# Optimization experiments

Measured on AMD Instinct MI355X. Metric: run time of the kernel, lower is better.

The kernel has to match this reference:

```python
import jax, jax.numpy as jnp
import numpy as np

HEADS = 16
EMBED = 1024
HEAD_DIM = EMBED // HEADS

def _split_heads(x):
    b, n, _ = x.shape
    return x.reshape(b, n, HEADS, HEAD_DIM).transpose(0, 2, 1, 3)  # b h n d

def _merge_heads(x):
    b, h, n, d = x.shape
    return x.transpose(0, 2, 1, 3).reshape(b, n, h * d)

def _attn(q_in, kv_in, Wq, bq, Wk, bk, Wv, bv, Wo, bo):
    q = _split_heads(q_in @ Wq + bq)
    k = _split_heads(kv_in @ Wk + bk)
    v = _split_heads(kv_in @ Wv + bv)
    e = jnp.einsum('bhqd,bhkd->bhqk', q, k) * (HEAD_DIM ** -0.5)
    a = jax.nn.softmax(e, axis=-1)
    o = jnp.einsum('bhqk,bhkd->bhqd', a, v)
    return _merge_heads(o) @ Wo + bo

def _layernorm(x, g, b, eps=1e-5):
    mu = jnp.mean(x, axis=-1, keepdims=True)
    var = jnp.var(x, axis=-1, keepdims=True)
    return (x - mu) * jax.lax.rsqrt(var + eps) * g + b

def setup_inputs() -> dict:
    key = jax.random.key(0)
    ks = jax.random.split(key, 20)
    s = 0.02
    d = {
        'temp_features': jax.random.normal(ks[0], (2, 2048, EMBED), jnp.float32),
        'spat_features': jax.random.normal(ks[1], (2, 2048, EMBED), jnp.float32),
    }
    names = ['t2s_Wq', 't2s_Wk', 't2s_Wv', 't2s_Wo', 's2t_Wq', 's2t_Wk', 's2t_Wv', 's2t_Wo']
    for i, nm in enumerate(names):
        d[nm] = jax.random.normal(ks[2 + i], (EMBED, EMBED), jnp.float32) * s
        d[nm.replace('W', 'b')] = jnp.zeros((EMBED,), jnp.float32)
    d['ln_g'] = jnp.ones((EMBED,), jnp.float32)
    d['ln_b'] = jnp.zeros((EMBED,), jnp.float32)
    return d

def reference(temp_features, spat_features,
              t2s_Wq, t2s_bq, t2s_Wk, t2s_bk, t2s_Wv, t2s_bv, t2s_Wo, t2s_bo,
              s2t_Wq, s2t_bq, s2t_Wk, s2t_bk, s2t_Wv, s2t_bv, s2t_Wo, s2t_bo,
              ln_g, ln_b):
    # t2s: queries from spat, keys/values from temp; residual = spat
    t2s = _attn(spat_features, temp_features, t2s_Wq, t2s_bq, t2s_Wk, t2s_bk,
                t2s_Wv, t2s_bv, t2s_Wo, t2s_bo)
    t2s_out = _layernorm(spat_features + t2s, ln_g, ln_b)
    # s2t: queries from temp, keys/values from spat; residual = temp
    s2t = _attn(temp_features, spat_features, s2t_Wq, s2t_bq, s2t_Wk, s2t_bk,
                s2t_Wv, s2t_bv, s2t_Wo, s2t_bo)
    s2t_out = _layernorm(temp_features + s2t, ln_g, ln_b)
    return (s2t_out, t2s_out)
```

## Files before the change

kernel.cpp:

```cpp
#include <hip/hip_runtime.h>
#include <stdint.h>

#define SEQ 2048
#define EMB 1024
#define NROWS 4096

typedef __bf16 bf16x8 __attribute__((ext_vector_type(8)));
typedef float f32x4 __attribute__((ext_vector_type(4)));
typedef unsigned short ushort8 __attribute__((ext_vector_type(8)));

__device__ __forceinline__ unsigned short f2bf(float f) {
  unsigned int u = __float_as_uint(f);
  u += 0x7fffu + ((u >> 16) & 1u);
  return (unsigned short)(u >> 16);
}

__device__ __forceinline__ float bf2f(unsigned short h) {
  return __uint_as_float((unsigned int)h << 16);
}

__device__ __forceinline__ f32x4 mfma16(bf16x8 a, bf16x8 b, f32x4 c) {
  return __builtin_amdgcn_mfma_f32_16x16x32_bf16(a, b, c, 0, 0, 0);
}

__device__ __forceinline__ void async_load16(const void* g, void* l) {
  auto gp = reinterpret_cast<__attribute__((address_space(1))) void*>(
      reinterpret_cast<uintptr_t>(g));
  auto lp = reinterpret_cast<__attribute__((address_space(3))) void*>(
      reinterpret_cast<uintptr_t>(l));
  __builtin_amdgcn_global_load_lds(gp, lp, 16, 0, 0);
}

__global__ __launch_bounds__(256) void prep(const float* __restrict__ t,
                                            const float* __restrict__ s,
                                            unsigned short* __restrict__ tb,
                                            unsigned short* __restrict__ sb,
                                            const float* __restrict__ W0,
                                            const float* __restrict__ W1,
                                            const float* __restrict__ W2,
                                            const float* __restrict__ W3,
                                            const float* __restrict__ W4,
                                            const float* __restrict__ W5,
                                            const float* __restrict__ W6,
                                            const float* __restrict__ W7,
                                            unsigned short* __restrict__ Wt) {
  const int bx = blockIdx.x;
  if (bx < 8192) {
    int i = bx * 256 + threadIdx.x;
    const float* x; unsigned short* y;
    if (i < NROWS * EMB / 4) { x = t; y = tb; }
    else { x = s; y = sb; i -= NROWS * EMB / 4; }
    float4 v = ((const float4*)x)[i];
    ushort4 o;
    o.x = f2bf(v.x); o.y = f2bf(v.y); o.z = f2bf(v.z); o.w = f2bf(v.w);
    ((ushort4*)y)[i] = o;
    return;
  }
  const int e = bx - 8192;
  const int z = e >> 8, tt = e & 255;
  const float* Ws[8] = {W0, W1, W2, W3, W4, W5, W6, W7};
  const float* W = Ws[z];
  unsigned short* dst = Wt + ((size_t)z << 20);
  __shared__ unsigned short tile[64][65];
  const int n0 = (tt & 15) * 64, k0 = (tt >> 4) * 64;
#pragma unroll
  for (int i = 0; i < 16; ++i) {
    const int ee = i * 256 + threadIdx.x;
    const int kk = ee >> 6, nn = ee & 63;
    tile[kk][nn] = f2bf(W[(size_t)(k0 + kk) * EMB + n0 + nn]);
  }
  __syncthreads();
#pragma unroll
  for (int i = 0; i < 16; ++i) {
    const int ee = i * 256 + threadIdx.x;
    const int nn = ee >> 6, kk = ee & 63;
    dst[(size_t)(n0 + nn) * EMB + k0 + kk] = tile[kk][nn];
  }
}

__device__ __forceinline__ void gemm_core64(const unsigned short* __restrict__ A,
                                            const unsigned short* __restrict__ Bt,
                                            int m0, int bt0,
                                            unsigned short* As, unsigned short* Bs,
                                            f32x4 (&acc)[4][4]) {
  const int tid = threadIdx.x;
  const int w = tid >> 6, lane = tid & 63;
  const int quad = lane >> 4, l16 = lane & 15;
  const int wm = w & 1, wn = w >> 1;
  const int sw8 = l16 & 7;

  const int srow = lane >> 3, p8 = lane & 7;
  const unsigned short* Ag[4];
  const unsigned short* Bg[4];
#pragma unroll
  for (int i = 0; i < 4; ++i) {
    const int r = w * 32 + i * 8 + srow;
    Ag[i] = A + (size_t)(m0 + r) * EMB + ((p8 ^ (r & 7)) * 8);
    Bg[i] = Bt + (size_t)(bt0 + r) * EMB + ((p8 ^ (r & 7)) * 8);
  }
  unsigned short* AsB[4];
  unsigned short* BsB[4];
#pragma unroll
  for (int i = 0; i < 4; ++i) {
    AsB[i] = As + (w * 32 + i * 8) * 64;
    BsB[i] = Bs + (w * 32 + i * 8) * 64;
  }

  for (int kk = 0; kk < EMB; kk += 64) {
    __syncthreads();
#pragma unroll
    for (int i = 0; i < 4; ++i) {
      async_load16(Ag[i] + kk, AsB[i]);
      async_load16(Bg[i] + kk, BsB[i]);
    }
    __syncthreads();
#pragma unroll
    for (int h = 0; h < 2; ++h) {
      bf16x8 af[4], bfr[4];
#pragma unroll
      for (int im = 0; im < 4; ++im)
        af[im] = *(const bf16x8*)(As + (wm * 64 + im * 16 + l16) * 64 +
                                  (((h * 4 + quad) ^ sw8) * 8));
#pragma unroll
      for (int in = 0; in < 4; ++in)
        bfr[in] = *(const bf16x8*)(Bs + (wn * 64 + in * 16 + l16) * 64 +
                                   (((h * 4 + quad) ^ sw8) * 8));
#pragma unroll
      for (int im = 0; im < 4; ++im)
#pragma unroll
        for (int in = 0; in < 4; ++in)
          acc[im][in] = mfma16(af[im], bfr[in], acc[im][in]);
    }
  }
}

__global__ __launch_bounds__(256, 3) void gemm_qkv(const unsigned short* __restrict__ tempb,
                                                   const unsigned short* __restrict__ spatb,
                                                   const unsigned short* __restrict__ Wt,
                                                   const float* __restrict__ bq0,
                                                   const float* __restrict__ bk0,
                                                   const float* __restrict__ bv0,
                                                   const float* __restrict__ bq1,
                                                   const float* __restrict__ bk1,
                                                   const float* __restrict__ bv1,
                                                   unsigned short* __restrict__ Qb,
                                                   unsigned short* __restrict__ Kb,
                                                   unsigned short* __restrict__ Vtb) {
  __shared__ alignas(16) unsigned short As[128 * 64];
  __shared__ alignas(16) unsigned short Bs[128 * 64];
  const int idx = blockIdx.x >> 3;
  const int dir = idx / 3, kind = idx - dir * 3;
  const int n0 = (blockIdx.x & 7) * 128;
  const unsigned short* A =
      (dir == 0) ? (kind == 0 ? tempb : spatb) : (kind == 0 ? spatb : tempb);
  const float* bias = (dir == 0) ? (kind == 0 ? bq0 : (kind == 1 ? bk0 : bv0))
                                 : (kind == 0 ? bq1 : (kind == 1 ? bk1 : bv1));

  f32x4 acc[4][4] = {};
  gemm_core64(A, Wt + ((size_t)(dir * 4 + kind) << 20), blockIdx.y * 128, n0, As, Bs, acc);

  const int tid = threadIdx.x;
  const int w = tid >> 6, lane = tid & 63;
  const int quad = lane >> 4, l16 = lane & 15;
  const int wm = w & 1, wn = w >> 1;
  const int rowb = blockIdx.y * 128 + wm * 64;
  const size_t dof = (size_t)dir * NROWS * EMB;

  if (kind == 2) {
    unsigned short* Vt = Vtb + dof;
#pragma unroll
    for (int in = 0; in < 4; ++in) {
      const int col = n0 + wn * 64 + in * 16 + l16;
      const int h = col >> 6, d = col & 63;
      const float bvv = bias[col];
#pragma unroll
      for (int im = 0; im < 4; ++im) {
        const int row = rowb + im * 16 + quad * 4;
        const int b = row >> 11, key = row & 2047;
        ushort4 o;
        o.x = f2bf(acc[im][in][0] + bvv);
        o.y = f2bf(acc[im][in][1] + bvv);
        o.z = f2bf(acc[im][in][2] + bvv);
        o.w = f2bf(acc[im][in][3] + bvv);
        *(ushort4*)(Vt + ((size_t)(b * 16 + h) * 64 + d) * SEQ + key) = o;
      }
    }
  } else {
    unsigned short* out = ((kind == 0) ? Qb : Kb) + dof;
    const float scale = (kind == 0) ? 0.18033688011112042f : 1.0f;
#pragma unroll
    for (int in = 0; in < 4; ++in) {
      const int col = n0 + wn * 64 + in * 16 + l16;
      const float bvv = bias[col];
#pragma unroll
      for (int im = 0; im < 4; ++im)
#pragma unroll
        for (int r = 0; r < 4; ++r) {
          const int row = rowb + im * 16 + quad * 4 + r;
          out[(size_t)row * EMB + col] = f2bf((acc[im][in][r] + bvv) * scale);
        }
    }
  }
}

__global__ __launch_bounds__(256, 3) void gemm_o(const unsigned short* __restrict__ Ob,
                                                 const unsigned short* __restrict__ Wt,
                                                 const float* __restrict__ bo0,
                                                 const float* __restrict__ bo1,
                                                 const float* __restrict__ temp,
                                                 const float* __restrict__ spat,
                                                 unsigned short* __restrict__ projb) {
  __shared__ alignas(16) unsigned short As[128 * 64];
  __shared__ alignas(16) unsigned short Bs[128 * 64];
  const int dir = blockIdx.x >> 3;
  const int n0 = (blockIdx.x & 7) * 128;
  const size_t dof = (size_t)dir * NROWS * EMB;
  const float* bias = dir ? bo1 : bo0;
  const float* resid = dir ? spat : temp;

  f32x4 acc[4][4] = {};
  gemm_core64(Ob + dof, Wt + ((size_t)(dir * 4 + 3) << 20), blockIdx.y * 128, n0, As, Bs,
              acc);

  const int tid = threadIdx.x;
  const int w = tid >> 6, lane = tid & 63;
  const int quad = lane >> 4, l16 = lane & 15;
  const int wm = w & 1, wn = w >> 1;
  const int rowb = blockIdx.y * 128 + wm * 64;
  unsigned short* outb = projb + dof;
#pragma unroll
  for (int in = 0; in < 4; ++in) {
    const int col = n0 + wn * 64 + in * 16 + l16;
    const float bvv = bias[col];
#pragma unroll
    for (int im = 0; im < 4; ++im)
#pragma unroll
      for (int r = 0; r < 4; ++r) {
        const int row = rowb + im * 16 + quad * 4 + r;
        const size_t off = (size_t)row * EMB + col;
        outb[off] = f2bf(acc[im][in][r] + bvv + resid[off]);
      }
  }
}

__global__ __launch_bounds__(256, 4) void flash_attn(const unsigned short* __restrict__ Qall,
                                                     const unsigned short* __restrict__ Kall,
                                                     const unsigned short* __restrict__ Vtall,
                                                     unsigned short* __restrict__ Oall) {
  __shared__ alignas(16) unsigned short Ks[2][64 * 64];
  __shared__ alignas(16) unsigned short Vs[64 * 64];
  __shared__ alignas(16) unsigned short Ps[4][2048];

  const int tid = threadIdx.x;
  const int w = tid >> 6, lane = tid & 63;
  const int quad = lane >> 4, l16 = lane & 15;
  const int phys = blockIdx.x + (blockIdx.y << 4);
  const int xcd = phys & 7, slot = phys >> 3;
  const int bxv = slot & 15;
  const int byv = (xcd << 3) + (slot >> 4);
  const int dir = byv >> 5, bh = byv & 31;
  const int b = bh >> 4, h = bh & 15;
  const size_t dof = (size_t)dir * NROWS * EMB;
  const unsigned short* Q = Qall + dof;
  const unsigned short* K = Kall + dof;
  const unsigned short* Vt = Vtall + dof;
  unsigned short* O = Oall + dof;
  const int q0 = bxv * 128 + w * 32;

  bf16x8 qf[2][2];
#pragma unroll
  for (int qh = 0; qh < 2; ++qh) {
    const unsigned short* Qrow = Q + (size_t)(b * SEQ + q0 + qh * 16 + l16) * EMB + h * 64;
    qf[qh][0] = *(const bf16x8*)(Qrow + quad * 8);
    qf[qh][1] = *(const bf16x8*)(Qrow + 32 + quad * 8);
  }

  bf16x8 onesf;
#pragma unroll
  for (int i = 0; i < 8; ++i) onesf[i] = (__bf16)1.0f;

  f32x4 oaccT[2][4] = {};
  f32x4 rs[2] = {};
  unsigned short* pw = &Ps[w][0];
  const int swz = (l16 & 7) << 1;
  const int sw8 = l16 & 7;

  const int r8 = lane >> 3, p8 = lane & 7;
  const int kr0 = w * 16 + r8, kr1 = kr0 + 8;
  const unsigned short* Ksrc0 = K + (size_t)(b * SEQ + kr0) * EMB + h * 64 + ((p8 ^ (kr0 & 7)) * 8);
  const unsigned short* Ksrc1 = K + (size_t)(b * SEQ + kr1) * EMB + h * 64 + ((p8 ^ (kr1 & 7)) * 8);
  const unsigned short* Vsrc0 = Vt + ((size_t)bh * 64 + kr0) * SEQ + ((p8 ^ (kr0 & 7)) * 8);
  const unsigned short* Vsrc1 = Vt + ((size_t)bh * 64 + kr1) * SEQ + ((p8 ^ (kr1 & 7)) * 8);
  unsigned short* KsW0 = &Ks[0][0] + (w * 16) * 64;
  unsigned short* KsW1 = &Ks[0][0] + (w * 16 + 8) * 64;
  unsigned short* VsW0 = Vs + (w * 16) * 64;
  unsigned short* VsW1 = Vs + (w * 16 + 8) * 64;

  async_load16(Ksrc0, KsW0);
  async_load16(Ksrc1, KsW1);
  async_load16(Vsrc0, VsW0);
  async_load16(Vsrc1, VsW1);
  asm volatile("s_waitcnt vmcnt(0)" ::: "memory");
  __builtin_amdgcn_s_barrier();
  asm volatile("" ::: "memory");

  int cur = 0;
  for (int kt = 0; kt < SEQ; kt += 64) {
    const bool more = (kt + 64 < SEQ);
    const int nb = cur ^ 1;
    if (more) {
      async_load16(Ksrc0 + (size_t)(kt + 64) * EMB, KsW0 + nb * 4096);
      async_load16(Ksrc1 + (size_t)(kt + 64) * EMB, KsW1 + nb * 4096);
    }

    const unsigned short* KsC = &Ks[cur][0];

#pragma unroll
    for (int g = 0; g < 4; ++g) {
      const int key = g * 16 + l16;
      bf16x8 kf0 = *(const bf16x8*)(KsC + key * 64 + ((quad ^ sw8) * 8));
      bf16x8 kf1 = *(const bf16x8*)(KsC + key * 64 + (((4 + quad) ^ sw8) * 8));
      const int kb = 4 * g + quad;
#pragma unroll
      for (int qh = 0; qh < 2; ++qh) {
        f32x4 z = {};
        z = mfma16(kf0, qf[qh][0], z);
        z = mfma16(kf1, qf[qh][1], z);
        uint2 pk;
        pk.x = (__float_as_uint(__builtin_amdgcn_exp2f(z[0])) >> 16) |
               (__float_as_uint(__builtin_amdgcn_exp2f(z[1])) & 0xffff0000u);
        pk.y = (__float_as_uint(__builtin_amdgcn_exp2f(z[2])) >> 16) |
               (__float_as_uint(__builtin_amdgcn_exp2f(z[3])) & 0xffff0000u);
        *(uint2*)(pw + (qh * 16 + l16) * 64 + ((kb ^ swz) << 2)) = pk;
      }
    }
    asm volatile("" ::: "memory");
    bf16x8 pb[2][2];
#pragma unroll
    for (int qh = 0; qh < 2; ++qh) {
      const int qrow = qh * 16 + l16;
      pb[qh][0] = *(const bf16x8*)(pw + qrow * 64 + (((2 * quad) ^ swz) << 2));
      pb[qh][1] = *(const bf16x8*)(pw + qrow * 64 + (((8 + 2 * quad) ^ swz) << 2));
      rs[qh] = mfma16(onesf, pb[qh][1], mfma16(onesf, pb[qh][0], rs[qh]));
    }
    asm volatile("" ::: "memory");

    if (more) asm volatile("s_waitcnt vmcnt(2)" ::: "memory");
    else      asm volatile("s_waitcnt vmcnt(0)" ::: "memory");
    __builtin_amdgcn_s_barrier();
    asm volatile("" ::: "memory");

#pragma unroll
    for (int dg = 0; dg < 4; ++dg) {
      const int dd = dg * 16 + l16;
      bf16x8 v0 = *(const bf16x8*)(Vs + dd * 64 + ((quad ^ sw8) * 8));
      bf16x8 v1 = *(const bf16x8*)(Vs + dd * 64 + (((4 + quad) ^ sw8) * 8));
#pragma unroll
      for (int qh = 0; qh < 2; ++qh) {
        oaccT[qh][dg] = mfma16(v0, pb[qh][0], oaccT[qh][dg]);
        oaccT[qh][dg] = mfma16(v1, pb[qh][1], oaccT[qh][dg]);
      }
    }
    asm volatile("" ::: "memory");

    if (more) {
      __builtin_amdgcn_s_barrier();
      async_load16(Vsrc0 + (kt + 64), VsW0);
      async_load16(Vsrc1 + (kt + 64), VsW1);
      asm volatile("s_waitcnt vmcnt(2)" ::: "memory");
      __builtin_amdgcn_s_barrier();
      asm volatile("" ::: "memory");
    }
    cur ^= 1;
  }

#pragma unroll
  for (int qh = 0; qh < 2; ++qh) {
    const float inv = 1.0f / rs[qh][0];
#pragma unroll
    for (int dg = 0; dg < 4; ++dg) {
      uint2 pk;
      pk.x = (unsigned int)f2bf(oaccT[qh][dg][0] * inv) |
             ((unsigned int)f2bf(oaccT[qh][dg][1] * inv) << 16);
      pk.y = (unsigned int)f2bf(oaccT[qh][dg][2] * inv) |
             ((unsigned int)f2bf(oaccT[qh][dg][3] * inv) << 16);
      const int kb = 4 * dg + quad;
      *(uint2*)(pw + l16 * 64 + ((kb ^ swz) << 2)) = pk;
    }
    asm volatile("" ::: "memory");
    const int qq = lane >> 2, cc = lane & 3;
    const int swq = (qq & 7) << 1;
    ushort8 r0 = *(const ushort8*)(pw + qq * 64 + (((4 * cc) ^ swq) << 2));
    ushort8 r1 = *(const ushort8*)(pw + qq * 64 + (((4 * cc + 2) ^ swq) << 2));
    unsigned short* Orow = O + (size_t)(b * SEQ + q0 + qh * 16 + qq) * EMB + h * 64 + cc * 16;
    *(ushort8*)(Orow) = r0;
    *(ushort8*)(Orow + 8) = r1;
    asm volatile("" ::: "memory");
  }
}

__global__ __launch_bounds__(256) void ln_k(const unsigned short* __restrict__ X,
                                            const float* __restrict__ g,
                                            const float* __restrict__ bb,
                                            float* __restrict__ out) {
  const int row = blockIdx.x;
  const int tid = threadIdx.x;
  const ushort4 hv = ((const ushort4*)(X + (size_t)row * EMB))[tid];
  float4 v;
  v.x = bf2f(hv.x); v.y = bf2f(hv.y); v.z = bf2f(hv.z); v.w = bf2f(hv.w);
  float s = v.x + v.y + v.z + v.w;
  float s2 = v.x * v.x + v.y * v.y + v.z * v.z + v.w * v.w;
#pragma unroll
  for (int o = 32; o > 0; o >>= 1) {
    s += __shfl_down(s, o);
    s2 += __shfl_down(s2, o);
  }
  __shared__ float ws[4], ws2[4];
  if ((tid & 63) == 0) { ws[tid >> 6] = s; ws2[tid >> 6] = s2; }
  __syncthreads();
  const float S = ws[0] + ws[1] + ws[2] + ws[3];
  const float S2 = ws2[0] + ws2[1] + ws2[2] + ws2[3];
  const float mu = S * (1.f / EMB);
  const float inv = rsqrtf(S2 * (1.f / EMB) - mu * mu + 1e-5f);
  const float4 gv = ((const float4*)g)[tid];
  const float4 bv = ((const float4*)bb)[tid];
  float4 o4;
  o4.x = (v.x - mu) * inv * gv.x + bv.x;
  o4.y = (v.y - mu) * inv * gv.y + bv.y;
  o4.z = (v.z - mu) * inv * gv.z + bv.z;
  o4.w = (v.w - mu) * inv * gv.w + bv.w;
  ((float4*)(out + (size_t)row * EMB))[tid] = o4;
}

extern "C" void kernel_launch(void* const* d_in, const int* in_sizes, int n_in,
                              void* d_out, int out_size, void* d_ws, size_t ws_size,
                              hipStream_t stream) {
  const float* temp = (const float*)d_in[0];
  const float* spat = (const float*)d_in[1];
  const float* lng = (const float*)d_in[18];
  const float* lnb = (const float*)d_in[19];
  float* out = (float*)d_out;

  char* base = (char*)d_ws;
  unsigned short* tempb = (unsigned short*)(base + ((size_t)0 << 20));
  unsigned short* spatb = (unsigned short*)(base + ((size_t)8 << 20));
  unsigned short* Wt = (unsigned short*)(base + ((size_t)16 << 20));
  unsigned short* Qb = (unsigned short*)(base + ((size_t)32 << 20));
  unsigned short* Kb = (unsigned short*)(base + ((size_t)48 << 20));
  unsigned short* Vtb = (unsigned short*)(base + ((size_t)64 << 20));
  unsigned short* Ob = (unsigned short*)(base + ((size_t)80 << 20));
  unsigned short* projb = (unsigned short*)(base + ((size_t)32 << 20));

  prep<<<8192 + 2048, 256, 0, stream>>>(
      temp, spat, tempb, spatb, (const float*)d_in[10], (const float*)d_in[12],
      (const float*)d_in[14], (const float*)d_in[16], (const float*)d_in[2],
      (const float*)d_in[4], (const float*)d_in[6], (const float*)d_in[8], Wt);
  gemm_qkv<<<dim3(48, 32), 256, 0, stream>>>(
      tempb, spatb, Wt, (const float*)d_in[11], (const float*)d_in[13],
      (const float*)d_in[15], (const float*)d_in[3], (const float*)d_in[5],
      (const float*)d_in[7], Qb, Kb, Vtb);
  flash_attn<<<dim3(16, 64), 256, 0, stream>>>(Qb, Kb, Vtb, Ob);
  gemm_o<<<dim3(16, 32), 256, 0, stream>>>(Ob, Wt, (const float*)d_in[17],
                                           (const float*)d_in[9], temp, spat, projb);
  ln_k<<<2 * NROWS, 256, 0, stream>>>(projb, lng, lnb, out);
}
```

Baseline: 306.6 us.

## Keep softmax probabilities in registers by permuting K rows at load time

Rather than writing exp'd scores to shared memory and reading them back as MFMA B operands, the kernel permutes which global key rows land in each LDS K slot. The QK^T output fragments then already match the operand layout needed for the PV MFMA, so they are packed directly into bf16x8 registers. This removes an LDS write/read round trip and its ordering fences on every key tile. It relies on the key permutation matching the V row order, which is a correctness risk if the mapping is off.

New measurement: 315.1 us. 1.03x slower.

```diff
diff --git a/kernel.cpp b/kernel.cpp
--- a/kernel.cpp
+++ b/kernel.cpp
@@ -21,6 +21,12 @@
 
 __device__ __forceinline__ f32x4 mfma16(bf16x8 a, bf16x8 b, f32x4 c) {
   return __builtin_amdgcn_mfma_f32_16x16x32_bf16(a, b, c, 0, 0, 0);
+}
+
+__device__ __forceinline__ bf16x8 pk2_to_bf16x8(uint2 a, uint2 b) {
+  union { unsigned int u[4]; bf16x8 v; } t;
+  t.u[0] = a.x; t.u[1] = a.y; t.u[2] = b.x; t.u[3] = b.y;
+  return t.v;
 }
 
 __device__ __forceinline__ void async_load16(const void* g, void* l) {
@@ -286,9 +292,12 @@
   const int sw8 = l16 & 7;
 
   const int r8 = lane >> 3, p8 = lane & 7;
-  const int kr0 = w * 16 + r8, kr1 = kr0 + 8;
-  const unsigned short* Ksrc0 = K + (size_t)(b * SEQ + kr0) * EMB + h * 64 + ((p8 ^ (kr0 & 7)) * 8);
-  const unsigned short* Ksrc1 = K + (size_t)(b * SEQ + kr1) * EMB + h * 64 + ((p8 ^ (kr1 & 7)) * 8);
+  const int gk0 = ((w >> 1) << 5) + ((r8 >> 2) << 3) + ((w & 1) << 2) + (r8 & 3);
+  const int gk1 = gk0 + 16;
+  const int kr0 = w * 16 + r8;
+  const int kr1 = kr0 + 8;
+  const unsigned short* Ksrc0 = K + (size_t)(b * SEQ + gk0) * EMB + h * 64 + ((p8 ^ r8) * 8);
+  const unsigned short* Ksrc1 = K + (size_t)(b * SEQ + gk1) * EMB + h * 64 + ((p8 ^ r8) * 8);
   const unsigned short* Vsrc0 = Vt + ((size_t)bh * 64 + kr0) * SEQ + ((p8 ^ (kr0 & 7)) * 8);
   const unsigned short* Vsrc1 = Vt + ((size_t)bh * 64 + kr1) * SEQ + ((p8 ^ (kr1 & 7)) * 8);
   unsigned short* KsW0 = &Ks[0][0] + (w * 16) * 64;
@@ -315,35 +324,32 @@
 
     const unsigned short* KsC = &Ks[cur][0];
 
+    uint2 pk[2][4];
 #pragma unroll
     for (int g = 0; g < 4; ++g) {
-      const int key = g * 16 + l16;
-      bf16x8 kf0 = *(const bf16x8*)(KsC + key * 64 + ((quad ^ sw8) * 8));
-      bf16x8 kf1 = *(const bf16x8*)(KsC + key * 64 + (((4 + quad) ^ sw8) * 8));
-      const int kb = 4 * g + quad;
+      const int krow = g * 16 + l16;
+      bf16x8 kf0 = *(const bf16x8*)(KsC + krow * 64 + ((quad ^ sw8) * 8));
+      bf16x8 kf1 = *(const bf16x8*)(KsC + krow * 64 + (((4 + quad) ^ sw8) * 8));
 #pragma unroll
       for (int qh = 0; qh < 2; ++qh) {
         f32x4 z = {};
         z = mfma16(kf0, qf[qh][0], z);
         z = mfma16(kf1, qf[qh][1], z);
-        uint2 pk;
-        pk.x = (__float_as_uint(__builtin_amdgcn_exp2f(z[0])) >> 16) |
-               (__float_as_uint(__builtin_amdgcn_exp2f(z[1])) & 0xffff0000u);
-        pk.y = (__float_as_uint(__builtin_amdgcn_exp2f(z[2])) >> 16) |
-               (__float_as_uint(__builtin_amdgcn_exp2f(z[3])) & 0xffff0000u);
-        *(uint2*)(pw + (qh * 16 + l16) * 64 + ((kb ^ swz) << 2)) = pk;
+        uint2 t;
+        t.x = (__float_as_uint(__builtin_amdgcn_exp2f(z[0])) >> 16) |
+              (__float_as_uint(__builtin_amdgcn_exp2f(z[1])) & 0xffff0000u);
+        t.y = (__float_as_uint(__builtin_amdgcn_exp2f(z[2])) >> 16) |
+              (__float_as_uint(__builtin_amdgcn_exp2f(z[3])) & 0xffff0000u);
+        pk[qh][g] = t;
       }
     }
-    asm volatile("" ::: "memory");
     bf16x8 pb[2][2];
 #pragma unroll
     for (int qh = 0; qh < 2; ++qh) {
-      const int qrow = qh * 16 + l16;
-      pb[qh][0] = *(const bf16x8*)(pw + qrow * 64 + (((2 * quad) ^ swz) << 2));
-      pb[qh][1] = *(const bf16x8*)(pw + qrow * 64 + (((8 + 2 * quad) ^ swz) << 2));
+      pb[qh][0] = pk2_to_bf16x8(pk[qh][0], pk[qh][1]);
+      pb[qh][1] = pk2_to_bf16x8(pk[qh][2], pk[qh][3]);
       rs[qh] = mfma16(onesf, pb[qh][1], mfma16(onesf, pb[qh][0], rs[qh]));
     }
-    asm volatile("" ::: "memory");
 
     if (more) asm volatile("s_waitcnt vmcnt(2)" ::: "memory");
     else      asm volatile("s_waitcnt vmcnt(0)" ::: "memory");
@@ -379,13 +385,13 @@
     const float inv = 1.0f / rs[qh][0];
 #pragma unroll
     for (int dg = 0; dg < 4; ++dg) {
-      uint2 pk;
-      pk.x = (unsigned int)f2bf(oaccT[qh][dg][0] * inv) |
-             ((unsigned int)f2bf(oaccT[qh][dg][1] * inv) << 16);
-      pk.y = (unsigned int)f2bf(oaccT[qh][dg][2] * inv) |
-             ((unsigned int)f2bf(oaccT[qh][dg][3] * inv) << 16);
+      uint2 pkk;
+      pkk.x = (unsigned int)f2bf(oaccT[qh][dg][0] * inv) |
+              ((unsigned int)f2bf(oaccT[qh][dg][1] * inv) << 16);
+      pkk.y = (unsigned int)f2bf(oaccT[qh][dg][2] * inv) |
+              ((unsigned int)f2bf(oaccT[qh][dg][3] * inv) << 16);
       const int kb = 4 * dg + quad;
-      *(uint2*)(pw + l16 * 64 + ((kb ^ swz) << 2)) = pk;
+      *(uint2*)(pw + l16 * 64 + ((kb ^ swz) << 2)) = pkk;
     }
     asm volatile("" ::: "memory");
     const int qq = lane >> 2, cc = lane & 3;
```
